# Kernel tuning notes

Hardware: AMD Instinct MI355X
Metric: run time of the kernel (lower is better)

## Reference

```python
import jax, jax.numpy as jnp
import numpy as np

B, T, N, C = 32, 12, 1024, 64
NW = T - 3  # number of temporal windows / conv output length


def setup_inputs() -> dict:
    key = jax.random.key(0)
    ks = jax.random.split(key, 10)
    return {
        "data": jax.random.normal(ks[0], (B, T, N, C), jnp.float32),
        "adj": jax.random.uniform(ks[1], (4 * N, 4 * N), jnp.float32) / (4.0 * N),
        "temporal_emb": jax.random.normal(ks[2], (1, T, 1, C), jnp.float32) * 0.05,
        "spatial_emb": jax.random.normal(ks[3], (1, 1, N, C), jnp.float32) * 0.05,
        "conv_wl": jax.random.normal(ks[4], (C, C, 1, 2), jnp.float32) * 0.05,
        "conv_bl": jnp.zeros((C,), jnp.float32),
        "conv_wr": jax.random.normal(ks[5], (C, C, 1, 2), jnp.float32) * 0.05,
        "conv_br": jnp.zeros((C,), jnp.float32),
        "fc_w": jax.random.normal(ks[6], (NW, 3, C, 2 * C), jnp.float32) * 0.05,
        "fc_b": jnp.zeros((NW, 3, 2 * C), jnp.float32),
    }


def reference(data, adj, temporal_emb, spatial_emb, conv_wl, conv_bl, conv_wr, conv_br, fc_w, fc_b):
    Bs, Ts, Ns, Cs = data.shape
    nw = Ts - 3
    x = data + temporal_emb + spatial_emb  # [B,T,N,C]

    # Gated dilated temporal conv: Conv2d kernel (1,2), dilation (1,3) over time
    # out[b,t,n,o] = sum_c w[o,c,0,0]*x[b,t,n,c] + w[o,c,0,1]*x[b,t+3,n,c] + b[o]
    def dconv(w, b):
        return (jnp.einsum('btnc,oc->btno', x[:, :nw], w[:, :, 0, 0])
                + jnp.einsum('btnc,oc->btno', x[:, 3:], w[:, :, 0, 1]) + b)

    data_res = jax.nn.sigmoid(dconv(conv_wl, conv_bl)) * jnp.tanh(dconv(conv_wr, conv_br))  # [B,nw,N,C]

    # Sliding windows of 4 time steps -> [nw, B, 4N, C]
    wins = jnp.stack([x[:, i:i + 4].reshape(Bs, 4 * Ns, Cs) for i in range(nw)], axis=0)

    F = fc_w.shape[-1] // 2  # GLU filter size

    def stsgcm(xw, Ws, bs):
        # xw: [B,4N,C]; Ws: [3,Cin,2F]; bs: [3,2F]
        h = xw
        outs = []
        for k in range(Ws.shape[0]):
            h = jnp.einsum('vw,bwc->bvc', adj, h)       # graph aggregation
            g = h @ Ws[k] + bs[k]                        # linear
            h = g[..., :F] * jax.nn.sigmoid(g[..., F:])  # GLU
            outs.append(h[:, Ns:2 * Ns])                 # middle vertex block
        return jnp.max(jnp.stack(outs, axis=0), axis=0)  # [B,N,F]

    spatial = jax.vmap(stsgcm)(wins, fc_w, fc_b)  # [nw,B,N,F]
    return spatial.transpose(1, 0, 2, 3) + data_res
```

## Files before the change

kernel.cpp:

```cpp
#include <hip/hip_runtime.h>
#include <math.h>

typedef unsigned char  u8;
typedef unsigned short u16;
typedef unsigned int   u32;
typedef __attribute__((ext_vector_type(8))) short bf16x8;
typedef __attribute__((ext_vector_type(8))) int   i32x8;
typedef __attribute__((ext_vector_type(4))) float f32x4;

typedef const void __attribute__((address_space(1))) gv1_t;
typedef void       __attribute__((address_space(3))) lv3_t;
#define GLL(g, l) __builtin_amdgcn_global_load_lds((gv1_t*)(g), (lv3_t*)(l), 16, 0, 0)

__device__ __forceinline__ u16 f2b(float x) {
    union { float f; u32 u; } v; v.f = x;
    u32 r = v.u + 0x7FFFu + ((v.u >> 16) & 1u);
    return (u16)(r >> 16);
}
__device__ __forceinline__ float b2f(u32 x) {
    union { u32 u; float f; } v; v.u = x << 16;
    return v.f;
}
__device__ __forceinline__ float fast_sigmoid(float x) {
    return __builtin_amdgcn_rcpf(1.0f + __builtin_amdgcn_exp2f(-x * 1.44269504f));
}
__device__ __forceinline__ float fast_tanh(float x) {
    return 2.0f * __builtin_amdgcn_rcpf(1.0f + __builtin_amdgcn_exp2f(-x * 2.88539008f)) - 1.0f;
}

__device__ __forceinline__ u8 f2e4m3(float x) {
    union { float f; u32 u; } v; v.f = x;
    u32 s = (v.u >> 24) & 0x80u;
    u32 a = v.u & 0x7fffffffu;
    if (a >= 0x43d80000u) return (u8)(s | 0x7e);
    if (a >= 0x3c800000u) {
        u32 expf = a >> 23;
        u32 keep = (a >> 20) & 7u;
        u32 rest = a & 0xfffffu;
        u32 vv = ((expf - 120u) << 3) | keep;
        vv += (rest > 0x80000u) || ((rest == 0x80000u) && (keep & 1u));
        return (u8)(s | vv);
    }
    float t = fabsf(x) * 512.0f;
    u32 ti = (u32)(t + 0.5f);
    return (u8)(s | ti);
}
__device__ __forceinline__ float e4m3f(u32 b) {
    u32 e = (b >> 3) & 15u, m = b & 7u;
    union { u32 u; float f; } t;
    t.u = ((e + 120u) << 23) | (m << 20);
    float v = e ? t.f : ((float)m * 0.001953125f);
    return (b & 0x80u) ? -v : v;
}


__global__ void cvt_adj_fp8(const float* __restrict__ a, u8* __restrict__ o, int n) {
    for (int i = (blockIdx.x * 256 + threadIdx.x) * 4; i < n; i += gridDim.x * 256 * 4) {
        float4 v = *(const float4*)&a[i];
        u32 pk = (u32)f2e4m3(v.x * 8192.0f) | ((u32)f2e4m3(v.y * 8192.0f) << 8)
               | ((u32)f2e4m3(v.z * 8192.0f) << 16) | ((u32)f2e4m3(v.w * 8192.0f) << 24);
        int row = i >> 12;
        int addr = (i & ~127) | (((((i >> 4) & 7) ^ (row & 7)) << 4)) | (i & 15);
        *(u32*)&o[addr] = pk;
    }
}

__global__ void prep_x(const float* __restrict__ data, const float* __restrict__ temb,
                       const float* __restrict__ semb, u16* __restrict__ Xn, u8* __restrict__ XT) {
    const int n0 = blockIdx.x * 64, t = blockIdx.y, b = blockIdx.z;
    const int tid = threadIdx.x;
    __shared__ u16 lt[64][66];
#pragma unroll
    for (int p = 0; p < 4; p++) {
        int n = p * 16 + (tid >> 4);
        int c = (tid & 15) * 4;
        size_t gi = ((size_t)(b * 12 + t) * 1024 + n0 + n) * 64 + c;
        float4 v  = *(const float4*)&data[gi];
        float4 tv = *(const float4*)&temb[t * 64 + c];
        float4 sv = *(const float4*)&semb[(n0 + n) * 64 + c];
        u16 u0 = f2b(v.x + tv.x + sv.x);
        u16 u1 = f2b(v.y + tv.y + sv.y);
        u16 u2 = f2b(v.z + tv.z + sv.z);
        u16 u3 = f2b(v.w + tv.w + sv.w);
        uint2 pk; pk.x = (u32)u0 | ((u32)u1 << 16); pk.y = (u32)u2 | ((u32)u3 << 16);
        *(uint2*)&Xn[gi] = pk;
        lt[n][c + 0] = u0; lt[n][c + 1] = u1; lt[n][c + 2] = u2; lt[n][c + 3] = u3;
    }
    __syncthreads();
    const int c = tid >> 2, q = tid & 3;
    u32 w[4];
#pragma unroll
    for (int i = 0; i < 4; i++) {
        u32 b0 = f2e4m3(b2f(lt[q * 16 + i * 4 + 0][c]));
        u32 b1 = f2e4m3(b2f(lt[q * 16 + i * 4 + 1][c]));
        u32 b2 = f2e4m3(b2f(lt[q * 16 + i * 4 + 2][c]));
        u32 b3 = f2e4m3(b2f(lt[q * 16 + i * 4 + 3][c]));
        w[i] = b0 | (b1 << 8) | (b2 << 16) | (b3 << 24);
    }
    const int row = b * 64 + c;
    size_t kk = (size_t)t * 1024 + n0 + q * 16;
    size_t seg = kk & ~(size_t)127;
    int chunk = (((int)(kk >> 4) & 7) ^ (row & 7));
    uint4 pk; pk.x = w[0]; pk.y = w[1]; pk.z = w[2]; pk.w = w[3];
    *(uint4*)&XT[(size_t)row * 12288 + seg + chunk * 16] = pk;
}

__global__ void prep_w(const float* __restrict__ fcw, const float* __restrict__ cwl,
                       const float* __restrict__ cwr, u16* __restrict__ Wt, u16* __restrict__ Wc) {
    const int blk = blockIdx.x, tid = threadIdx.x;
    if (blk < 27) {
        const float* src = fcw + (size_t)blk * 64 * 128;
        u16* dst = Wt + (size_t)blk * 128 * 64;
        for (int e = tid; e < 8192; e += 256) {
            int c = e >> 7, f = e & 127;
            dst[f * 64 + c] = f2b(src[c * 128 + f]);
        }
    } else {
        for (int e = tid; e < 16384; e += 256) {
            int o = e >> 7, k = e & 127;
            float v = (o < 64) ? cwl[(o * 64 + (k & 63)) * 2 + (k >> 6)]
                               : cwr[((o - 64) * 64 + (k & 63)) * 2 + (k >> 6)];
            Wc[o * 128 + k] = f2b(v);
        }
    }
}

__global__ __launch_bounds__(256) void dconv_gemm(
    const u16* __restrict__ Xn, const u16* __restrict__ Wc,
    const float* __restrict__ cbl, const float* __restrict__ cbr,
    float* __restrict__ out) {
    const int n0 = blockIdx.x * 128, t = blockIdx.y, b = blockIdx.z;
    const int tid = threadIdx.x, lane = tid & 63, wid = tid >> 6;
    __shared__ u16 alds[2][128 * 32];
    const u16* base0 = Xn + (size_t)(b * 12 + t) * 1024 * 64;
    const u16* base3 = Xn + (size_t)(b * 12 + t + 3) * 1024 * 64;

    auto stage = [&](int buf, int kt) {
        int k0 = kt * 32;
#pragma unroll
        for (int q = 0; q < 2; q++) {
            int r = wid * 32 + q * 16 + (lane >> 2);
            int k = k0 + (lane & 3) * 8;
            const u16* gs = (k < 64) ? base0 + (size_t)(n0 + r) * 64 + k
                                     : base3 + (size_t)(n0 + r) * 64 + (k - 64);
            GLL(gs, &alds[buf][(wid * 32 + q * 16) * 32]);
        }
    };

    f32x4 acc[2][8] = {};
    stage(0, 0);
    __syncthreads();
    const int a_off = (wid * 32 + (lane & 15)) * 32 + (lane >> 4) * 8;
    for (int kt = 0; kt < 4; kt++) {
        int cur = kt & 1;
        if (kt < 3) stage(cur ^ 1, kt + 1);
        bf16x8 af[2];
#pragma unroll
        for (int m = 0; m < 2; m++) af[m] = *(const bf16x8*)&alds[cur][a_off + m * 16 * 32];
#pragma unroll
        for (int n = 0; n < 8; n++) {
            bf16x8 bq = *(const bf16x8*)&Wc[(n * 16 + (lane & 15)) * 128 + kt * 32 + (lane >> 4) * 8];
#pragma unroll
            for (int m = 0; m < 2; m++)
                acc[m][n] = __builtin_amdgcn_mfma_f32_16x16x32_bf16(af[m], bq, acc[m][n], 0, 0, 0);
        }
        __syncthreads();
    }
#pragma unroll
    for (int m = 0; m < 2; m++) {
#pragma unroll
        for (int n = 0; n < 4; n++) {
            int fp = n * 16 + (lane & 15);
            float b1 = cbl[fp], b2 = cbr[fp];
#pragma unroll
            for (int j = 0; j < 4; j++) {
                int row = wid * 32 + m * 16 + (lane >> 4) * 4 + j;
                float gl = acc[m][n][j] + b1;
                float gr = acc[m][n + 4][j] + b2;
                out[((size_t)(b * 9 + t) * 1024 + n0 + row) * 64 + fp] =
                    fast_sigmoid(gl) * fast_tanh(gr);
            }
        }
    }
}

#define SCB() __builtin_amdgcn_sched_barrier(0)
#define BARR() do { SCB(); __builtin_amdgcn_s_barrier(); SCB(); } while (0)
#define WAITK0 do { asm volatile("s_waitcnt lgkmcnt(0)" ::: "memory"); SCB(); } while (0)
#define GATE8 do { SCB(); asm volatile("s_waitcnt vmcnt(8)" ::: "memory"); SCB(); } while (0)
#define GATEZ do { SCB(); asm volatile("s_waitcnt vmcnt(0)" ::: "memory"); SCB(); } while (0)

template <int STAGE>
__global__ __launch_bounds__(256, 2) void agg_mx(
    const u8* __restrict__ A, const u8* __restrict__ Bt,
    const u16* __restrict__ Wt, const float* __restrict__ fcb,
    u8* __restrict__ P, int win0, int vbase, int nout, int ks, float ysc) {
    const int tid = threadIdx.x, lane = tid & 63, wid = tid >> 6;
    const int wr = wid >> 1, wc = wid & 1;
    const u32 lin2 = blockIdx.x + gridDim.x * blockIdx.y;
    const u32 per = (gridDim.x * gridDim.y) >> 3;
    const u32 w2 = (lin2 & 7) * per + (lin2 >> 3);
    const int bx = w2 % gridDim.x;
    const int by = w2 / gridDim.x;
    const int z = blockIdx.z;
    const int rowBase = by * 128, colBase = bx * 128;
    const int win = win0 + z;
    __shared__ u8 ldsb[65536];
    __shared__ float biasSm[128];
    biasSm[tid & 127] = fcb[(win * 3 + ks) * 128 + (tid & 127)];
    const u8* Az = (STAGE == 0) ? (A + (size_t)win * 1024)
                                : (A + (size_t)z * 2048 * 4096);
    const size_t strideA = (STAGE == 0) ? 12288 : 4096;

    const int r8 = lane >> 3;
    const int c16 = (lane & 7) * 16;
    auto stageA = [&](int buf, int s, int kt) {
        int r_l = s * 32 + wid * 8;
        GLL(Az + (size_t)(rowBase + r_l + r8) * strideA + (size_t)kt * 128 + c16,
            &ldsb[buf * 32768 + r_l * 128]);
    };
    auto stageB = [&](int buf, int s, int kt) {
        int r_l = s * 32 + wid * 8;
        GLL(Bt + (size_t)(vbase + colBase + r_l + r8) * 4096 + (size_t)kt * 128 + c16,
            &ldsb[buf * 32768 + 16384 + r_l * 128]);
    };
#define STAGE8M(buf, kt) do { stageA(buf, 0, kt); stageA(buf, 1, kt); \
                              stageA(buf, 2, kt); stageA(buf, 3, kt); \
                              stageB(buf, 0, kt); stageB(buf, 1, kt); \
                              stageB(buf, 2, kt); stageB(buf, 3, kt); } while (0)

    f32x4 acc[4][4] = {};
    i32x8 fa[4], fb[4];
    const int q0 = lane >> 4;

#define RD_ABM(buf)                                                           \
    _Pragma("unroll") for (int mm = 0; mm < 4; mm++) {                        \
        int r = wr * 64 + mm * 16 + (lane & 15);                              \
        int h = r & 7;                                                        \
        const u8* bp = &ldsb[(buf) * 32768 + r * 128];                        \
        ((uint4*)&fa[mm])[0] = *(const uint4*)&bp[((2 * q0) ^ h) * 16];       \
        ((uint4*)&fa[mm])[1] = *(const uint4*)&bp[((2 * q0 + 1) ^ h) * 16];   \
    }                                                                         \
    _Pragma("unroll") for (int nn = 0; nn < 4; nn++) {                        \
        int r = wc * 64 + nn * 16 + (lane & 15);                              \
        int h = r & 7;                                                        \
        const u8* bp = &ldsb[(buf) * 32768 + 16384 + r * 128];                \
        ((uint4*)&fb[nn])[0] = *(const uint4*)&bp[((2 * q0) ^ h) * 16];       \
        ((uint4*)&fb[nn])[1] = *(const uint4*)&bp[((2 * q0 + 1) ^ h) * 16];   \
    }
#define MFMA16M()                                                             \
    __builtin_amdgcn_s_setprio(1);                                            \
    _Pragma("unroll") for (int mm = 0; mm < 4; mm++)                          \
    _Pragma("unroll") for (int nn = 0; nn < 4; nn++)                          \
        acc[mm][nn] = __builtin_amdgcn_mfma_scale_f32_16x16x128_f8f6f4(       \
            fa[mm], fb[nn], acc[mm][nn], 0, 0, 0, 127, 0, 127);               \
    __builtin_amdgcn_s_setprio(0);

#define TILE14M(RB, T2S) do {                                                 \
    BARR();                                                                   \
    RD_ABM(RB);                                                               \
    WAITK0;                                                                   \
    BARR();                                                                   \
    STAGE8M(RB, T2S);                                                         \
    SCB();                                                                    \
    MFMA16M();                                                                \
    GATE8;                                                                    \
} while (0)

    STAGE8M(0, 0);
    STAGE8M(1, 1);
    GATE8;

    for (int t = 0; t < 30; t += 2) {
        TILE14M(0, t + 2);
        TILE14M(1, t + 3);
    }
    BARR();
    RD_ABM(0);
    WAITK0;
    BARR();
    MFMA16M();
    GATEZ;
    BARR();
    RD_ABM(1);
    WAITK0;
    MFMA16M();

    __syncthreads();
    u16* YT = (u16*)ldsb;
#pragma unroll
    for (int mm = 0; mm < 4; mm++) {
        int c0 = mm * 16 + q0 * 4;
#pragma unroll
        for (int nn = 0; nn < 4; nn++) {
            int v = wc * 64 + nn * 16 + (lane & 15);
            ushort4 pk;
            pk.x = f2b(acc[mm][nn][0] * ysc); pk.y = f2b(acc[mm][nn][1] * ysc);
            pk.z = f2b(acc[mm][nn][2] * ysc); pk.w = f2b(acc[mm][nn][3] * ysc);
            int addr = (wr * 128 + v) * 64 + (((c0 >> 3) ^ (v & 7)) << 3) + (c0 & 7);
            *(ushort4*)&YT[addr] = pk;
        }
    }
    __syncthreads();

    const int bat = wid >> 1, fh = wid & 1;
    const u16* Wl = Wt + (size_t)(win * 3 + ks) * 8192;
    u8* Pz = P + (size_t)z * 2048 * nout;
    bf16x8 aw[4][2];
#pragma unroll
    for (int p = 0; p < 4; p++) {
        int mt = (p & 1) + fh * 2 + (p >> 1) * 4;
#pragma unroll
        for (int kk = 0; kk < 2; kk++)
            aw[p][kk] = *(const bf16x8*)&Wl[(mt * 16 + (lane & 15)) * 64 + kk * 32 + q0 * 8];
    }
#pragma unroll
    for (int vp = 0; vp < 4; vp++) {
        f32x4 acc2[4][2] = {};
        bf16x8 bq2[2][2];
#pragma unroll
        for (int nt = 0; nt < 2; nt++) {
            int v = vp * 32 + nt * 16 + (lane & 15);
#pragma unroll
            for (int kk = 0; kk < 2; kk++) {
                int ch = kk * 4 + q0;
                bq2[nt][kk] = *(const bf16x8*)&YT[(bat * 128 + v) * 64 + ((ch ^ (v & 7)) << 3)];
            }
        }
#pragma unroll
        for (int p = 0; p < 4; p++)
#pragma unroll
            for (int nt = 0; nt < 2; nt++)
#pragma unroll
                for (int kk = 0; kk < 2; kk++)
                    acc2[p][nt] = __builtin_amdgcn_mfma_f32_16x16x32_bf16(
                        aw[p][kk], bq2[nt][kk], acc2[p][nt], 0, 0, 0);
#pragma unroll
        for (int p = 0; p < 2; p++) {
            int mt = (p & 1) + fh * 2;
#pragma unroll
            for (int j = 0; j < 4; j++) {
                int f = mt * 16 + q0 * 4 + j;
                float b1 = biasSm[f], b2v = biasSm[f + 64];
                int row = rowBase + bat * 64 + f;
#pragma unroll
                for (int nt = 0; nt < 2; nt++) {
                    float g1 = acc2[p][nt][j] + b1;
                    float g2 = acc2[p + 2][nt][j] + b2v;
                    float val = g1 * fast_sigmoid(g2);
                    int colg = colBase + vp * 32 + nt * 16 + (lane & 15);
                    int seg = colg & ~127;
                    int chunk = (((colg >> 4) & 7) ^ (row & 7));
                    Pz[(size_t)row * nout + seg + chunk * 16 + (colg & 15)] =
                        f2e4m3(val * 512.0f);
                }
            }
        }
    }
#undef RD_ABM
#undef MFMA16M
#undef TILE14M
#undef STAGE8M
}

__device__ __forceinline__ uint4 ld_swz(const u8* p, size_t rowBytes, size_t k, int h) {
    size_t seg = k & ~(size_t)127;
    int chunk = ((int)(k >> 4) & 7) ^ h;
    return *(const uint4*)&p[rowBytes + seg + chunk * 16];
}

__global__ void final_add(const u8* __restrict__ P1, const u8* __restrict__ P2,
                          const u8* __restrict__ P3, float* __restrict__ out, int win0) {
    const int n0 = blockIdx.x * 64, b = blockIdx.y, z = blockIdx.z;
    const int win = win0 + z;
    const int tid = threadIdx.x;
    __shared__ float tl[64][65];
    {
        int f = tid >> 2, q = tid & 3;
        int row = b * 64 + f;
        int h = row & 7;
        size_t rb12 = ((size_t)z * 2048 + row) * 4096;
        size_t rb3  = ((size_t)z * 2048 + row) * 1024;
        uint4 a  = ld_swz(P1, rb12, (size_t)1024 + n0 + q * 16, h);
        uint4 c2 = ld_swz(P2, rb12, (size_t)1024 + n0 + q * 16, h);
        uint4 d  = ld_swz(P3, rb3, (size_t)n0 + q * 16, h);
        const u32 aw[4] = {a.x, a.y, a.z, a.w};
        const u32 bw[4] = {c2.x, c2.y, c2.z, c2.w};
        const u32 dw[4] = {d.x, d.y, d.z, d.w};
#pragma unroll
        for (int w = 0; w < 4; w++)
#pragma unroll
            for (int j = 0; j < 4; j++) {
                float va = e4m3f((aw[w] >> (j * 8)) & 0xffu);
                float vb = e4m3f((bw[w] >> (j * 8)) & 0xffu);
                float vd = e4m3f((dw[w] >> (j * 8)) & 0xffu);
                tl[q * 16 + w * 4 + j][f] = fmaxf(fmaxf(va, vb), vd) * (1.0f / 512.0f);
            }
    }
    __syncthreads();
    {
        int n = tid >> 2, q = tid & 3;
        size_t oo = ((size_t)(b * 9 + win) * 1024 + n0 + n) * 64 + q * 16;
#pragma unroll
        for (int i = 0; i < 16; i += 4) {
            float4 cur = *(const float4*)&out[oo + i];
            cur.x += tl[n][q * 16 + i + 0];
            cur.y += tl[n][q * 16 + i + 1];
            cur.z += tl[n][q * 16 + i + 2];
            cur.w += tl[n][q * 16 + i + 3];
            *(float4*)&out[oo + i] = cur;
        }
    }
}

extern "C" void kernel_launch(void* const* d_in, const int* in_sizes, int n_in,
                              void* d_out, int out_size, void* d_ws, size_t ws_size,
                              hipStream_t stream) {
    const float* data = (const float*)d_in[0];
    const float* adj  = (const float*)d_in[1];
    const float* temb = (const float*)d_in[2];
    const float* semb = (const float*)d_in[3];
    const float* cwl  = (const float*)d_in[4];
    const float* cbl  = (const float*)d_in[5];
    const float* cwr  = (const float*)d_in[6];
    const float* cbr  = (const float*)d_in[7];
    const float* fcw  = (const float*)d_in[8];
    const float* fcb  = (const float*)d_in[9];
    float* out = (float*)d_out;

    const float YS1 = 1.0f / 8192.0f;
    const float YS2 = 1.0f / 4194304.0f;

    char* p = (char*)d_ws;
    auto alloc = [&](size_t bytes) -> char* {
        char* r = p;
        p += (bytes + 255) & ~(size_t)255;
        return r;
    };
    const size_t SZ_XT  = 2048UL * 12288;
    const size_t SZ_XN  = 32UL * 12 * 1024 * 64 * 2;
    const size_t SZ_ADJ = 4096UL * 4096;
    const size_t SZ_WT  = 27UL * 128 * 64 * 2;
    const size_t SZ_WC  = 128UL * 128 * 2;
    const size_t SZ_P12 = 2048UL * 4096;
    const size_t SZ_P3  = 2048UL * 1024;
    u8*  XT   = (u8*)alloc(SZ_XT);
    u8*  adjb = (u8*)alloc(SZ_ADJ);
    u16* Wt   = (u16*)alloc(SZ_WT);
    u16* Wc   = (u16*)alloc(SZ_WC);
    size_t fixed = (size_t)(p - (char*)d_ws);

    bool single = (fixed + 9 * (2 * SZ_P12) + SZ_XN + 1024 <= ws_size);
    if (single) {
        u8* P1 = (u8*)alloc(9 * SZ_P12);
        u8* P2 = (u8*)alloc(9 * SZ_P12);
        u8* P3 = XT;
        u16* Xn = (u16*)P2;

        cvt_adj_fp8<<<4096, 256, 0, stream>>>(adj, adjb, 4096 * 4096);
        prep_x<<<dim3(16, 12, 32), 256, 0, stream>>>(data, temb, semb, Xn, XT);
        prep_w<<<28, 256, 0, stream>>>(fcw, cwl, cwr, Wt, Wc);
        dconv_gemm<<<dim3(8, 9, 32), 256, 0, stream>>>(Xn, Wc, cbl, cbr, out);

        agg_mx<0><<<dim3(32, 16, 9), 256, 0, stream>>>(XT, adjb, Wt, fcb, P1, 0, 0, 4096, 0, YS1);
        agg_mx<1><<<dim3(32, 16, 9), 256, 0, stream>>>(P1, adjb, Wt, fcb, P2, 0, 0, 4096, 1, YS2);
        agg_mx<1><<<dim3(8, 16, 9), 256, 0, stream>>>(P2, adjb, Wt, fcb, P3, 0, 1024, 1024, 2, YS2);
        final_add<<<dim3(16, 32, 9), 256, 0, stream>>>(P1, P2, P3, out, 0);
    } else {
        char* winBase = p;
        size_t avail = ws_size - (size_t)(winBase - (char*)d_ws);
        const size_t perwin = 2 * SZ_P12 + SZ_P3 + 3 * 256;
        int cap = (int)(avail / perwin);
        if (cap > 9) cap = 9;
        if (cap < 1) cap = 1;
        u8* P1 = (u8*)alloc((size_t)cap * SZ_P12);
        u8* P2 = (u8*)alloc((size_t)cap * SZ_P12);
        u8* P3 = (u8*)alloc((size_t)cap * SZ_P3);
        u16* Xn = ((size_t)cap * perwin >= SZ_XN + 256) ? (u16*)winBase : (u16*)alloc(SZ_XN);

        cvt_adj_fp8<<<4096, 256, 0, stream>>>(adj, adjb, 4096 * 4096);
        prep_x<<<dim3(16, 12, 32), 256, 0, stream>>>(data, temb, semb, Xn, XT);
        prep_w<<<28, 256, 0, stream>>>(fcw, cwl, cwr, Wt, Wc);
        dconv_gemm<<<dim3(8, 9, 32), 256, 0, stream>>>(Xn, Wc, cbl, cbr, out);

        int ngroups = (9 + cap - 1) / cap;
        int gbase = 9 / ngroups, grem = 9 % ngroups;
        int w0 = 0;
        for (int g = 0; g < ngroups; g++) {
            int cw = gbase + (g < grem ? 1 : 0);
            agg_mx<0><<<dim3(32, 16, cw), 256, 0, stream>>>(XT, adjb, Wt, fcb, P1, w0, 0, 4096, 0, YS1);
            agg_mx<1><<<dim3(32, 16, cw), 256, 0, stream>>>(P1, adjb, Wt, fcb, P2, w0, 0, 4096, 1, YS2);
            agg_mx<1><<<dim3(8, 16, cw), 256, 0, stream>>>(P2, adjb, Wt, fcb, P3, w0, 1024, 1024, 2, YS2);
            final_add<<<dim3(16, 32, cw), 256, 0, stream>>>(P1, P2, P3, out, w0);
            w0 += cw;
        }
    }
}
```

Measured before the change: 1.029 ms.

## Double-buffer MFMA fragments in registers and drop XCD block swizzle

The fp8 aggregation GEMM main loop is restructured so that each phase reads the next LDS tile into a second set of register fragments while MFMAs run on the current set. This is meant to hide LDS read latency behind matrix math. The global-to-LDS prefetch now waits for all outstanding loads every phase, and the tail issues a redundant wrapped load (kt masked to 31). The XCD-aware block index remapping is also removed in favour of plain blockIdx, which may change L2 locality. Doubling the fragment registers raises register pressure under the 256x2 launch bound.

New measurement: 1.063 ms. +3.4%, slower.

```diff
diff --git a/kernel.cpp b/kernel.cpp
--- a/kernel.cpp
+++ b/kernel.cpp
@@ -186,8 +186,8 @@
 
 #define SCB() __builtin_amdgcn_sched_barrier(0)
 #define BARR() do { SCB(); __builtin_amdgcn_s_barrier(); SCB(); } while (0)
-#define WAITK0 do { asm volatile("s_waitcnt lgkmcnt(0)" ::: "memory"); SCB(); } while (0)
-#define GATE8 do { SCB(); asm volatile("s_waitcnt vmcnt(8)" ::: "memory"); SCB(); } while (0)
+#define WAITK15 do { SCB(); asm volatile("s_waitcnt lgkmcnt(15)" ::: "memory"); SCB(); } while (0)
+#define WAITK0  do { SCB(); asm volatile("s_waitcnt lgkmcnt(0)"  ::: "memory"); SCB(); } while (0)
 #define GATEZ do { SCB(); asm volatile("s_waitcnt vmcnt(0)" ::: "memory"); SCB(); } while (0)
 
 template <int STAGE>
@@ -197,12 +197,7 @@
     u8* __restrict__ P, int win0, int vbase, int nout, int ks, float ysc) {
     const int tid = threadIdx.x, lane = tid & 63, wid = tid >> 6;
     const int wr = wid >> 1, wc = wid & 1;
-    const u32 lin2 = blockIdx.x + gridDim.x * blockIdx.y;
-    const u32 per = (gridDim.x * gridDim.y) >> 3;
-    const u32 w2 = (lin2 & 7) * per + (lin2 >> 3);
-    const int bx = w2 % gridDim.x;
-    const int by = w2 / gridDim.x;
-    const int z = blockIdx.z;
+    const int bx = blockIdx.x, by = blockIdx.y, z = blockIdx.z;
     const int rowBase = by * 128, colBase = bx * 128;
     const int win = win0 + z;
     __shared__ u8 ldsb[65536];
@@ -215,11 +210,13 @@
     const int r8 = lane >> 3;
     const int c16 = (lane & 7) * 16;
     auto stageA = [&](int buf, int s, int kt) {
+        kt &= 31;
         int r_l = s * 32 + wid * 8;
         GLL(Az + (size_t)(rowBase + r_l + r8) * strideA + (size_t)kt * 128 + c16,
             &ldsb[buf * 32768 + r_l * 128]);
     };
     auto stageB = [&](int buf, int s, int kt) {
+        kt &= 31;
         int r_l = s * 32 + wid * 8;
         GLL(Bt + (size_t)(vbase + colBase + r_l + r8) * 4096 + (size_t)kt * 128 + c16,
             &ldsb[buf * 32768 + 16384 + r_l * 128]);
@@ -230,61 +227,56 @@
                               stageB(buf, 2, kt); stageB(buf, 3, kt); } while (0)
 
     f32x4 acc[4][4] = {};
-    i32x8 fa[4], fb[4];
+    i32x8 fa[2][4], fb[2][4];
     const int q0 = lane >> 4;
 
-#define RD_ABM(buf)                                                           \
+#define RD_SET(S, BUF)                                                        \
     _Pragma("unroll") for (int mm = 0; mm < 4; mm++) {                        \
         int r = wr * 64 + mm * 16 + (lane & 15);                              \
         int h = r & 7;                                                        \
-        const u8* bp = &ldsb[(buf) * 32768 + r * 128];                        \
-        ((uint4*)&fa[mm])[0] = *(const uint4*)&bp[((2 * q0) ^ h) * 16];       \
-        ((uint4*)&fa[mm])[1] = *(const uint4*)&bp[((2 * q0 + 1) ^ h) * 16];   \
+        const u8* bp = &ldsb[(BUF) * 32768 + r * 128];                        \
+        ((uint4*)&fa[S][mm])[0] = *(const uint4*)&bp[((2 * q0) ^ h) * 16];    \
+        ((uint4*)&fa[S][mm])[1] = *(const uint4*)&bp[((2 * q0 + 1) ^ h) * 16];\
     }                                                                         \
     _Pragma("unroll") for (int nn = 0; nn < 4; nn++) {                        \
         int r = wc * 64 + nn * 16 + (lane & 15);                              \
         int h = r & 7;                                                        \
-        const u8* bp = &ldsb[(buf) * 32768 + 16384 + r * 128];                \
-        ((uint4*)&fb[nn])[0] = *(const uint4*)&bp[((2 * q0) ^ h) * 16];       \
-        ((uint4*)&fb[nn])[1] = *(const uint4*)&bp[((2 * q0 + 1) ^ h) * 16];   \
-    }
-#define MFMA16M()                                                             \
+        const u8* bp = &ldsb[(BUF) * 32768 + 16384 + r * 128];                \
+        ((uint4*)&fb[S][nn])[0] = *(const uint4*)&bp[((2 * q0) ^ h) * 16];    \
+        ((uint4*)&fb[S][nn])[1] = *(const uint4*)&bp[((2 * q0 + 1) ^ h) * 16];\
+    }
+#define MFMA_SET(S)                                                           \
     __builtin_amdgcn_s_setprio(1);                                            \
     _Pragma("unroll") for (int mm = 0; mm < 4; mm++)                          \
     _Pragma("unroll") for (int nn = 0; nn < 4; nn++)                          \
         acc[mm][nn] = __builtin_amdgcn_mfma_scale_f32_16x16x128_f8f6f4(       \
-            fa[mm], fb[nn], acc[mm][nn], 0, 0, 0, 127, 0, 127);               \
+            fa[S][mm], fb[S][nn], acc[mm][nn], 0, 0, 0, 127, 0, 127);         \
     __builtin_amdgcn_s_setprio(0);
 
-#define TILE14M(RB, T2S) do {                                                 \
+#define PHASE(CUR, NXT, T) do {                                               \
+    RD_SET(NXT, NXT);                                                         \
+    WAITK15;                                                                  \
     BARR();                                                                   \
-    RD_ABM(RB);                                                               \
-    WAITK0;                                                                   \
+    STAGE8M(CUR, (T) + 2);                                                    \
+    SCB();                                                                    \
+    MFMA_SET(CUR);                                                            \
+    GATEZ;                                                                    \
     BARR();                                                                   \
-    STAGE8M(RB, T2S);                                                         \
-    SCB();                                                                    \
-    MFMA16M();                                                                \
-    GATE8;                                                                    \
 } while (0)
 
     STAGE8M(0, 0);
     STAGE8M(1, 1);
-    GATE8;
-
-    for (int t = 0; t < 30; t += 2) {
-        TILE14M(0, t + 2);
-        TILE14M(1, t + 3);
-    }
-    BARR();
-    RD_ABM(0);
-    WAITK0;
-    BARR();
-    MFMA16M();
     GATEZ;
     BARR();
-    RD_ABM(1);
+    RD_SET(0, 0);
+
+    for (int i = 0; i < 15; i++) {
+        PHASE(0, 1, 2 * i);
+        PHASE(1, 0, 2 * i + 1);
+    }
+    PHASE(0, 1, 30);
     WAITK0;
-    MFMA16M();
+    MFMA_SET(1);
 
     __syncthreads();
     u16* YT = (u16*)ldsb;
@@ -357,9 +349,9 @@
             }
         }
     }
-#undef RD_ABM
-#undef MFMA16M
-#undef TILE14M
+#undef RD_SET
+#undef MFMA_SET
+#undef PHASE
 #undef STAGE8M
 }
 
```
